# Kernel optimization log

Measured on AMD Instinct MI355X. Metric: run time of the kernel, lower is better.

The kernel has to match this reference:

```python
import jax, jax.numpy as jnp
import numpy as np

EMBED_DIM = 1024
NUM_HEADS = 16
HEAD_DIM = EMBED_DIM // NUM_HEADS


def setup_inputs() -> dict:
    key = jax.random.key(0)
    k_x, k_wqkv, k_bqkv, k_wo, k_bo = jax.random.split(key, 5)
    bound = 1.0 / np.sqrt(EMBED_DIM)
    x = jax.random.normal(k_x, (2, 2048, EMBED_DIM), dtype=jnp.float32)
    # torch Linear weight is [out, in]; store as [in, out] for x @ W
    W_qkv = jax.random.uniform(k_wqkv, (EMBED_DIM, 3 * EMBED_DIM), minval=-bound, maxval=bound, dtype=jnp.float32)
    b_qkv = jax.random.uniform(k_bqkv, (3 * EMBED_DIM,), minval=-bound, maxval=bound, dtype=jnp.float32)
    W_out = jax.random.uniform(k_wo, (EMBED_DIM, EMBED_DIM), minval=-bound, maxval=bound, dtype=jnp.float32)
    b_out = jax.random.uniform(k_bo, (EMBED_DIM,), minval=-bound, maxval=bound, dtype=jnp.float32)
    return {"x": x, "W_qkv": W_qkv, "b_qkv": b_qkv, "W_out": W_out, "b_out": b_out}


def reference(x, W_qkv, b_qkv, W_out, b_out):
    B, T, D = x.shape
    H, Hd = NUM_HEADS, HEAD_DIM
    qkv = x @ W_qkv + b_qkv                      # [B,T,3D]
    qkv = qkv.reshape(B, T, 3, H, Hd)
    q = qkv[:, :, 0].transpose(0, 2, 1, 3)       # [B,H,T,Hd]
    k = qkv[:, :, 1].transpose(0, 2, 1, 3)
    v = qkv[:, :, 2].transpose(0, 2, 1, 3)
    scores = jnp.einsum('bhqd,bhkd->bhqk', q, k) / jnp.sqrt(jnp.float32(Hd))
    attn = jax.nn.softmax(scores, axis=-1)       # [B,H,T,T]
    out = jnp.einsum('bhqk,bhkd->bhqd', attn, v) # [B,H,T,Hd]
    out = out.transpose(0, 2, 1, 3).reshape(B, T, D)
    return out @ W_out + b_out
```

## Files before the change

### kernel.cpp

```cpp
#include <hip/hip_runtime.h>
#include <hip/hip_bf16.h>

#define B_   2
#define T_   2048
#define D_   1024
#define H_   16
#define HD_  64
#define M_TOT (B_*T_)
#define N_QKV (3*D_)

typedef __attribute__((ext_vector_type(8))) short bf16x8;
typedef __attribute__((ext_vector_type(4))) float f32x4;
typedef __attribute__((ext_vector_type(16))) float f32x16;

static __device__ __forceinline__ short f2bf(float f) {
    union { __hip_bfloat16 h; short s; } u;
    u.h = __float2bfloat16(f);
    return u.s;
}
static __device__ __forceinline__ unsigned pack2(float a, float b) {
    return (unsigned)(unsigned short)f2bf(a) | ((unsigned)(unsigned short)f2bf(b) << 16);
}
static __device__ __forceinline__ float exp2_fast(float x) {
    return __builtin_amdgcn_exp2f(x);
}
static __device__ __forceinline__ f32x16 zero16() {
    f32x16 z;
    #pragma unroll
    for (int i = 0; i < 16; ++i) z[i] = 0.f;
    return z;
}
static __device__ __forceinline__ void gload16(const void* g, void* l) {
    __builtin_amdgcn_global_load_lds(
        (__attribute__((address_space(1))) unsigned int*)(unsigned long long)g,
        (__attribute__((address_space(3))) unsigned int*)l, 16, 0, 0);
}

__global__ __launch_bounds__(256) void convert_x(const float* __restrict__ x,
                                                 short* __restrict__ xb, int n8) {
    int i = blockIdx.x * blockDim.x + threadIdx.x;
    if (i >= n8) return;
    const float4* p = (const float4*)x + (size_t)i * 2;
    float4 a = p[0], b = p[1];
    bf16x8 o;
    o[0]=f2bf(a.x); o[1]=f2bf(a.y); o[2]=f2bf(a.z); o[3]=f2bf(a.w);
    o[4]=f2bf(b.x); o[5]=f2bf(b.y); o[6]=f2bf(b.z); o[7]=f2bf(b.w);
    *((bf16x8*)xb + i) = o;
}

__global__ __launch_bounds__(256) void transpose_convert(const float* __restrict__ in,
                                                         short* __restrict__ out,
                                                         int K, int N) {
    __shared__ short tile[64][65];
    int k0 = blockIdx.y * 64, n0 = blockIdx.x * 64;
    int t = threadIdx.x;
    #pragma unroll
    for (int i = 0; i < 16; ++i) {
        int idx = i * 256 + t;
        int r = idx >> 6, c = idx & 63;
        tile[r][c] = f2bf(in[(size_t)(k0 + r) * N + n0 + c]);
    }
    __syncthreads();
    #pragma unroll
    for (int i = 0; i < 16; ++i) {
        int idx = i * 256 + t;
        int r = idx >> 6, c = idx & 63;
        out[(size_t)(n0 + r) * K + k0 + c] = tile[c][r];
    }
}

#define QSC 0.18033688f
template<int BM, int BN, int MODE>
__global__ __launch_bounds__(256)
void gemm_dl(const short* __restrict__ A, const short* __restrict__ BT,
             const float* __restrict__ bias, int M, int N, int K,
             short* __restrict__ qo, short* __restrict__ ko,
             short* __restrict__ vo, float* __restrict__ fo) {
    constexpr int BUF = (BM + BN) * 128;
    __shared__ char smem[2 * BUF];
    const int t = threadIdx.x, w = t >> 6, l = t & 63;
    const int qi_l = l & 15, hi_l = l >> 4;

    const int nbx = gridDim.x, nwg = gridDim.x * gridDim.y;
    int f = blockIdx.y * nbx + blockIdx.x;
    f = (f & 7) * (nwg >> 3) + (f >> 3);
    const int m0 = (f / nbx) * BM, n0 = (f % nbx) * BN;

    const int wr = w >> 1, wc = w & 1;
    constexpr int MI = BM / 32, NI = BN / 32;

    f32x4 acc[MI][NI];
    #pragma unroll
    for (int mi = 0; mi < MI; ++mi)
        #pragma unroll
        for (int ni = 0; ni < NI; ++ni)
            acc[mi][ni] = (f32x4){0.f, 0.f, 0.f, 0.f};

    const int lrow = l >> 3;
    const int lch  = ((l & 7) ^ lrow) * 8;

    auto stage = [&](char* dst, int k0) {
        #pragma unroll
        for (int i = 0; i < BM / 32; ++i) {
            int rb = w * (BM / 4) + i * 8;
            gload16(A + (size_t)(m0 + rb + lrow) * K + k0 + lch, dst + rb * 128);
        }
        #pragma unroll
        for (int i = 0; i < BN / 32; ++i) {
            int rb = w * (BN / 4) + i * 8;
            gload16(BT + (size_t)(n0 + rb + lrow) * K + k0 + lch, dst + BM * 128 + rb * 128);
        }
    };

    stage(smem, 0);
    __syncthreads();

    int cur = 0;
    for (int k0 = 0; k0 < K; k0 += 64) {
        char* sA = smem + cur * BUF;
        char* sB = sA + BM * 128;
        if (k0 + 64 < K) stage(smem + (cur ^ 1) * BUF, k0 + 64);

        #pragma unroll
        for (int ks = 0; ks < 2; ++ks) {
            bf16x8 af[MI], bfr[NI];
            #pragma unroll
            for (int mi = 0; mi < MI; ++mi) {
                int row = wr * (BM / 2) + mi * 16 + qi_l;
                int ad = row * 128 + (((ks * 4 + hi_l) ^ (row & 7)) * 16);
                af[mi] = *(const bf16x8*)(sA + ad);
            }
            #pragma unroll
            for (int ni = 0; ni < NI; ++ni) {
                int row = wc * (BN / 2) + ni * 16 + qi_l;
                int ad = row * 128 + (((ks * 4 + hi_l) ^ (row & 7)) * 16);
                bfr[ni] = *(const bf16x8*)(sB + ad);
            }
            #pragma unroll
            for (int mi = 0; mi < MI; ++mi)
                #pragma unroll
                for (int ni = 0; ni < NI; ++ni)
                    acc[mi][ni] = __builtin_amdgcn_mfma_f32_16x16x32_bf16(af[mi], bfr[ni], acc[mi][ni], 0, 0, 0);
        }
        __syncthreads();
        cur ^= 1;
    }

    #pragma unroll
    for (int mi = 0; mi < MI; ++mi) {
        int rbase = m0 + wr * (BM / 2) + mi * 16 + 4 * hi_l;
        #pragma unroll
        for (int ni = 0; ni < NI; ++ni) {
            int n = n0 + wc * (BN / 2) + ni * 16 + qi_l;
            float bv = bias[n];
            #pragma unroll
            for (int r = 0; r < 4; ++r) {
                int mm = rbase + r;
                float c = acc[mi][ni][r] + bv;
                if (MODE == 0) {
                    int which = n >> 10, rest = n & 1023;
                    int h = rest >> 6, d = rest & 63;
                    int b = mm >> 11, tq = mm & 2047;
                    size_t bh = (size_t)(b * H_ + h);
                    if (which == 0)      qo[(bh * T_ + tq) * HD_ + d] = f2bf(c * QSC);
                    else if (which == 1) ko[(bh * T_ + tq) * HD_ + d] = f2bf(c);
                    else                 vo[(bh * HD_ + d) * T_ + tq] = f2bf(c);
                } else {
                    fo[(size_t)mm * N + n] = c;
                }
            }
        }
    }
}

__global__ __launch_bounds__(512)
void attn(const short* __restrict__ q, const short* __restrict__ k,
          const short* __restrict__ vt, short* __restrict__ ao) {
    __shared__ char smem[32768];

    const int t = threadIdx.x, w = t >> 6, l = t & 63;
    const int q32 = l & 31, hi2 = l >> 5;
    const int swz = (l & 7) << 4;
    const int bh = blockIdx.y;
    const int q0 = blockIdx.x * 256 + w * 32;

    const short* qptr = q + ((size_t)bh * T_ + q0) * HD_;
    const short* kbase = k + (size_t)bh * T_ * HD_;
    const short* vbase = vt + (size_t)bh * HD_ * T_;

    const int srow = w * 8 + (l >> 3);
    const int sch  = ((l & 7) ^ (l >> 3)) * 8;

    bf16x8 qa[4];
    #pragma unroll
    for (int kc = 0; kc < 4; ++kc)
        qa[kc] = *(const bf16x8*)(qptr + q32 * HD_ + kc * 16 + hi2 * 8);

    f32x16 o0 = zero16(), o1 = zero16();
    float m = -1e30f, lsum = 0.f;

    gload16(kbase + (size_t)srow * HD_ + sch, smem + srow * 128);
    gload16(vbase + (size_t)srow * T_ + sch,  smem + 8192 + srow * 128);
    __syncthreads();

    int cur = 0;
    for (int kb = 0; kb < T_; kb += 64) {
        char* sK = smem + cur * 16384;
        char* sV = sK + 8192;
        if (kb + 64 < T_) {
            char* nK = smem + (cur ^ 1) * 16384;
            gload16(kbase + (size_t)(kb + 64 + srow) * HD_ + sch, nK + srow * 128);
            gload16(vbase + (size_t)srow * T_ + (kb + 64) + sch,  nK + 8192 + srow * 128);
        }

        f32x16 s0 = zero16(), s1 = zero16();
        #pragma unroll
        for (int kc = 0; kc < 4; ++kc) {
            int off = (kc * 32 + hi2 * 16) ^ swz;
            bf16x8 kf0 = *(const bf16x8*)(sK + q32 * 128 + off);
            s0 = __builtin_amdgcn_mfma_f32_32x32x16_bf16(kf0, qa[kc], s0, 0, 0, 0);
            bf16x8 kf1 = *(const bf16x8*)(sK + (32 + q32) * 128 + off);
            s1 = __builtin_amdgcn_mfma_f32_32x32x16_bf16(kf1, qa[kc], s1, 0, 0, 0);
        }

        float a8[8];
        #pragma unroll
        for (int i = 0; i < 8; ++i)
            a8[i] = fmaxf(fmaxf(s0[i], s0[i + 8]), fmaxf(s1[i], s1[i + 8]));
        float b4_0 = fmaxf(a8[0], a8[1]), b4_1 = fmaxf(a8[2], a8[3]);
        float b4_2 = fmaxf(a8[4], a8[5]), b4_3 = fmaxf(a8[6], a8[7]);
        float tm = fmaxf(fmaxf(b4_0, b4_1), fmaxf(b4_2, b4_3));
        tm = fmaxf(tm, __shfl_xor(tm, 32));

        if (!__all(tm <= m + 8.f)) {
            float mnew = fmaxf(m, tm);
            float fsc = exp2_fast(m - mnew);
            lsum *= fsc;
            #pragma unroll
            for (int i = 0; i < 16; ++i) { o0[i] *= fsc; o1[i] *= fsc; }
            m = mnew;
        }

        #pragma unroll
        for (int i = 0; i < 16; ++i) {
            s0[i] = exp2_fast(s0[i] - m);
            s1[i] = exp2_fast(s1[i] - m);
        }
        float p8[8];
        #pragma unroll
        for (int i = 0; i < 8; ++i)
            p8[i] = (s0[i] + s0[i + 8]) + (s1[i] + s1[i + 8]);
        float psum = ((p8[0] + p8[1]) + (p8[2] + p8[3])) + ((p8[4] + p8[5]) + (p8[6] + p8[7]));
        psum += __shfl_xor(psum, 32);
        lsum += psum;

        unsigned pk0[8], pk1[8];
        #pragma unroll
        for (int p = 0; p < 8; ++p) {
            pk0[p] = pack2(s0[2 * p], s0[2 * p + 1]);
            pk1[p] = pack2(s1[2 * p], s1[2 * p + 1]);
        }

        #pragma unroll
        for (int c = 0; c < 4; ++c) {
            unsigned w0 = (c & 2) ? pk1[(c & 1) * 4 + 0] : pk0[(c & 1) * 4 + 0];
            unsigned w1 = (c & 2) ? pk1[(c & 1) * 4 + 1] : pk0[(c & 1) * 4 + 1];
            unsigned w2 = (c & 2) ? pk1[(c & 1) * 4 + 2] : pk0[(c & 1) * 4 + 2];
            unsigned w3 = (c & 2) ? pk1[(c & 1) * 4 + 3] : pk0[(c & 1) * 4 + 3];
            unsigned t0 = hi2 ? w0 : w2;
            unsigned t1 = hi2 ? w1 : w3;
            unsigned r0 = __shfl_xor(t0, 32);
            unsigned r1 = __shfl_xor(t1, 32);
            union { unsigned u[4]; bf16x8 v; } uf;
            uf.u[0] = hi2 ? r0 : w0;
            uf.u[1] = hi2 ? r1 : w1;
            uf.u[2] = hi2 ? w2 : r0;
            uf.u[3] = hi2 ? w3 : r1;
            bf16x8 pf = uf.v;

            int off = (c * 32 + hi2 * 16) ^ swz;
            bf16x8 vf0 = *(const bf16x8*)(sV + q32 * 128 + off);
            o0 = __builtin_amdgcn_mfma_f32_32x32x16_bf16(vf0, pf, o0, 0, 0, 0);
            bf16x8 vf1 = *(const bf16x8*)(sV + (32 + q32) * 128 + off);
            o1 = __builtin_amdgcn_mfma_f32_32x32x16_bf16(vf1, pf, o1, 0, 0, 0);
        }

        __syncthreads();
        cur ^= 1;
    }

    const float inv = 1.f / lsum;
    const int b = bh >> 4, h = bh & 15;
    const int tq = q0 + q32;
    unsigned* aou = (unsigned*)(ao + ((size_t)(b * T_ + tq)) * D_ + h * HD_);
    #pragma unroll
    for (int pr = 0; pr < 8; ++pr) {
        int d0 = 2 * (pr & 1) + 8 * (pr >> 1) + 4 * hi2;
        aou[d0 >> 1]        = pack2(o0[2 * pr] * inv, o0[2 * pr + 1] * inv);
        aou[(32 + d0) >> 1] = pack2(o1[2 * pr] * inv, o1[2 * pr + 1] * inv);
    }
}

extern "C" void kernel_launch(void* const* d_in, const int* in_sizes, int n_in,
                              void* d_out, int out_size, void* d_ws, size_t ws_size,
                              hipStream_t stream) {
    const float* x    = (const float*)d_in[0];
    const float* Wqkv = (const float*)d_in[1];
    const float* bqkv = (const float*)d_in[2];
    const float* Wout = (const float*)d_in[3];
    const float* bout = (const float*)d_in[4];
    float* out = (float*)d_out;

    char* ws = (char*)d_ws;
    short* xb  = (short*)(ws);
    short* WqT = (short*)(ws + ((size_t)8  << 20));
    short* WoT = (short*)(ws + ((size_t)14 << 20));
    short* qb  = (short*)(ws + ((size_t)16 << 20));
    short* kb  = (short*)(ws + ((size_t)24 << 20));
    short* vtb = (short*)(ws + ((size_t)32 << 20));
    short* aob = (short*)(ws + ((size_t)40 << 20));

    convert_x<<<(M_TOT * D_ / 8 + 255) / 256, 256, 0, stream>>>(x, xb, M_TOT * D_ / 8);
    transpose_convert<<<dim3(N_QKV / 64, D_ / 64), 256, 0, stream>>>(Wqkv, WqT, D_, N_QKV);
    transpose_convert<<<dim3(D_ / 64, D_ / 64), 256, 0, stream>>>(Wout, WoT, D_, D_);

    gemm_dl<128, 128, 0><<<dim3(N_QKV / 128, M_TOT / 128), 256, 0, stream>>>(
        xb, WqT, bqkv, M_TOT, N_QKV, D_, qb, kb, vtb, nullptr);

    attn<<<dim3(T_ / 256, B_ * H_), 512, 0, stream>>>(qb, kb, vtb, aob);

    gemm_dl<128, 64, 1><<<dim3(D_ / 64, M_TOT / 128), 256, 0, stream>>>(
        aob, WoT, bout, M_TOT, D_, D_, nullptr, nullptr, nullptr, out);
}
```

Measured before the change: 142.0 us.

## Issue next GEMM stage before waiting with vmcnt; shrink attention blocks to four waves

The GEMM loop now issues the next tile's global-to-LDS loads first, then waits with a partial s_waitcnt vmcnt so only the current tile's loads must be complete before the barrier. Full __syncthreads is replaced by raw s_barrier. The XCD-aware block index remapping is removed in favour of a plain grid mapping. The attention kernel moves from 512-thread blocks covering 256 queries to 256-thread blocks covering 128 queries, so each thread stages two K/V rows and the grid doubles. The intent is finer-grained load/compute overlap and better occupancy, at the risk of worse L2 locality without the swizzle and of ordering hazards with raw barriers.

```diff
diff --git a/kernel.cpp b/kernel.cpp
--- a/kernel.cpp
+++ b/kernel.cpp
@@ -77,15 +77,11 @@
              short* __restrict__ qo, short* __restrict__ ko,
              short* __restrict__ vo, float* __restrict__ fo) {
     constexpr int BUF = (BM + BN) * 128;
+    constexpr int NL = BM / 32 + BN / 32;
     __shared__ char smem[2 * BUF];
     const int t = threadIdx.x, w = t >> 6, l = t & 63;
     const int qi_l = l & 15, hi_l = l >> 4;
-
-    const int nbx = gridDim.x, nwg = gridDim.x * gridDim.y;
-    int f = blockIdx.y * nbx + blockIdx.x;
-    f = (f & 7) * (nwg >> 3) + (f >> 3);
-    const int m0 = (f / nbx) * BM, n0 = (f % nbx) * BN;
-
+    const int m0 = blockIdx.y * BM, n0 = blockIdx.x * BN;
     const int wr = w >> 1, wc = w & 1;
     constexpr int MI = BM / 32, NI = BN / 32;
 
@@ -113,14 +109,20 @@
     };
 
     stage(smem, 0);
-    __syncthreads();
-
     int cur = 0;
     for (int k0 = 0; k0 < K; k0 += 64) {
+        if (k0 + 64 < K) {
+            stage(smem + (cur ^ 1) * BUF, k0 + 64);
+            if constexpr (NL == 8)      asm volatile("s_waitcnt vmcnt(8)" ::: "memory");
+            else if constexpr (NL == 6) asm volatile("s_waitcnt vmcnt(6)" ::: "memory");
+            else                        asm volatile("s_waitcnt vmcnt(0)" ::: "memory");
+        } else {
+            asm volatile("s_waitcnt vmcnt(0)" ::: "memory");
+        }
+        __builtin_amdgcn_s_barrier();
+
         char* sA = smem + cur * BUF;
         char* sB = sA + BM * 128;
-        if (k0 + 64 < K) stage(smem + (cur ^ 1) * BUF, k0 + 64);
-
         #pragma unroll
         for (int ks = 0; ks < 2; ++ks) {
             bf16x8 af[MI], bfr[NI];
@@ -142,7 +144,7 @@
                 for (int ni = 0; ni < NI; ++ni)
                     acc[mi][ni] = __builtin_amdgcn_mfma_f32_16x16x32_bf16(af[mi], bfr[ni], acc[mi][ni], 0, 0, 0);
         }
-        __syncthreads();
+        __builtin_amdgcn_s_barrier();
         cur ^= 1;
     }
 
@@ -173,7 +175,7 @@
     }
 }
 
-__global__ __launch_bounds__(512)
+__global__ __launch_bounds__(256)
 void attn(const short* __restrict__ q, const short* __restrict__ k,
           const short* __restrict__ vt, short* __restrict__ ao) {
     __shared__ char smem[32768];
@@ -182,14 +184,14 @@
     const int q32 = l & 31, hi2 = l >> 5;
     const int swz = (l & 7) << 4;
     const int bh = blockIdx.y;
-    const int q0 = blockIdx.x * 256 + w * 32;
+    const int q0 = blockIdx.x * 128 + w * 32;
 
     const short* qptr = q + ((size_t)bh * T_ + q0) * HD_;
     const short* kbase = k + (size_t)bh * T_ * HD_;
     const short* vbase = vt + (size_t)bh * HD_ * T_;
 
-    const int srow = w * 8 + (l >> 3);
-    const int sch  = ((l & 7) ^ (l >> 3)) * 8;
+    const int sr = w * 8 + (l >> 3);
+    const int sch = ((l & 7) ^ (l >> 3)) * 8;
 
     bf16x8 qa[4];
     #pragma unroll
@@ -199,8 +201,12 @@
     f32x16 o0 = zero16(), o1 = zero16();
     float m = -1e30f, lsum = 0.f;
 
-    gload16(kbase + (size_t)srow * HD_ + sch, smem + srow * 128);
-    gload16(vbase + (size_t)srow * T_ + sch,  smem + 8192 + srow * 128);
+    #pragma unroll
+    for (int i = 0; i < 2; ++i) {
+        int r = i * 32 + sr;
+        gload16(kbase + (size_t)r * HD_ + sch, smem + r * 128);
+        gload16(vbase + (size_t)r * T_ + sch,  smem + 8192 + r * 128);
+    }
     __syncthreads();
 
     int cur = 0;
@@ -209,8 +215,12 @@
         char* sV = sK + 8192;
         if (kb + 64 < T_) {
             char* nK = smem + (cur ^ 1) * 16384;
-            gload16(kbase + (size_t)(kb + 64 + srow) * HD_ + sch, nK + srow * 128);
-            gload16(vbase + (size_t)srow * T_ + (kb + 64) + sch,  nK + 8192 + srow * 128);
+            #pragma unroll
+            for (int i = 0; i < 2; ++i) {
+                int r = i * 32 + sr;
+                gload16(kbase + (size_t)(kb + 64 + r) * HD_ + sch, nK + r * 128);
+                gload16(vbase + (size_t)r * T_ + (kb + 64) + sch,  nK + 8192 + r * 128);
+            }
         }
 
         f32x16 s0 = zero16(), s1 = zero16();
@@ -327,7 +337,7 @@
     gemm_dl<128, 128, 0><<<dim3(N_QKV / 128, M_TOT / 128), 256, 0, stream>>>(
         xb, WqT, bqkv, M_TOT, N_QKV, D_, qb, kb, vtb, nullptr);
 
-    attn<<<dim3(T_ / 256, B_ * H_), 512, 0, stream>>>(qb, kb, vtb, aob);
+    attn<<<dim3(T_ / 128, B_ * H_), 256, 0, stream>>>(qb, kb, vtb, aob);
 
     gemm_dl<128, 64, 1><<<dim3(D_ / 64, M_TOT / 128), 256, 0, stream>>>(
         aob, WoT, bout, M_TOT, D_, D_, nullptr, nullptr, nullptr, out);
```

New measurement: 147.3 us. +3.7%, slower.
